# Optimization experiments

Hardware: AMD Instinct MI355X
Metric: run time of the kernel (lower is better)

Reference implementation:

```python
import jax, jax.numpy as jnp
import numpy as np

N_NODES = 50000
N_EDGES = 800000
IN_DIM = 128
HID_DIM = 64


def gcn_conv(x, W, b, src, dst, ew):
    """PyG GCNConv with edge_weight: add self-loops (weight 1), symmetric
    normalization D^-1/2 (A+I) D^-1/2, linear transform, scatter-add, bias."""
    n = x.shape[0]
    loop = jnp.arange(n)
    src_a = jnp.concatenate([src, loop])           # [E+N]
    dst_a = jnp.concatenate([dst, loop])
    ew_a = jnp.concatenate([ew, jnp.ones((n,), dtype=x.dtype)])
    deg = jax.ops.segment_sum(ew_a, dst_a, num_segments=n)   # [N]
    dinv = jnp.where(deg > 0, jax.lax.rsqrt(deg), 0.0)
    norm = dinv[src_a] * ew_a * dinv[dst_a]        # [E+N]
    h = x @ W                                      # [N, out]
    msg = h[src_a] * norm[:, None]                 # gather + scale
    out = jax.ops.segment_sum(msg, dst_a, num_segments=n)    # scatter-add
    return out + b


def setup_inputs() -> dict:
    key = jax.random.key(0)
    k = jax.random.split(key, 6)
    x = jax.random.normal(k[0], (N_NODES, IN_DIM), dtype=jnp.float32)
    edge_index = jax.random.randint(k[1], (2, N_EDGES), 0, N_NODES, dtype=jnp.int64)
    edge_weight = jax.random.uniform(k[2], (N_EDGES,), dtype=jnp.float32)
    W1 = jax.random.normal(k[3], (IN_DIM, HID_DIM), dtype=jnp.float32) * (1.0 / np.sqrt(IN_DIM))
    b1 = jnp.zeros((HID_DIM,), dtype=jnp.float32)
    W2 = jax.random.normal(k[4], (HID_DIM, 1), dtype=jnp.float32) * (1.0 / np.sqrt(HID_DIM))
    b2 = jnp.zeros((1,), dtype=jnp.float32)
    return {"x": x, "edge_index": edge_index, "edge_weight": edge_weight,
            "W1": W1, "b1": b1, "W2": W2, "b2": b2}


def reference(x, edge_index, edge_weight, W1, b1, W2, b2):
    src, dst = edge_index[0], edge_index[1]
    h = gcn_conv(x, W1, b1, src, dst, edge_weight)
    h = jax.nn.relu(h)
    h = gcn_conv(h, W2, b2, src, dst, edge_weight)
    return jax.nn.sigmoid(h).squeeze(-1)           # [N]
```

## Files before the change

### kernel.cpp

```cpp
#include <hip/hip_runtime.h>
#include <hip/hip_bf16.h>
#include <math.h>

#define N_NODES 50000
#define N_EDGES 800000
#define IN_DIM  128
#define HID_DIM 64

#define NBKT     196
#define BKT_CAP  5000
#define NPASSC   200
#define EDGES_PER_PASSC (N_EDGES / NPASSC)
#define GEMM_NODES 64
#define NGEMM    782
#define XS_LD    132

__global__ __launch_bounds__(256)
void partgemm_kernel(const int* __restrict__ src, const int* __restrict__ dst,
                     const float* __restrict__ ew, int* __restrict__ gcursor,
                     int2* __restrict__ edge_b,
                     const float* __restrict__ x, const float* __restrict__ W1,
                     __hip_bfloat16* __restrict__ h1b) {
    __shared__ float w1s[IN_DIM * HID_DIM];
    __shared__ float xs[GEMM_NODES][XS_LD];
    int bid = blockIdx.x;
    int tid = threadIdx.x;
    if (bid < NPASSC) {
        int2*           epack = (int2*)w1s;
        unsigned short* ebkt  = (unsigned short*)&xs[0][0];
        int* cnt1    = (int*)(ebkt + EDGES_PER_PASSC);
        int* cnt2    = cnt1 + 256;
        int* runbase = cnt2 + 256;
        cnt1[tid] = 0; cnt2[tid] = 0;
        __syncthreads();
        int e0 = bid * EDGES_PER_PASSC;
        const int4*   s4p = (const int4*)(src + e0);
        const int4*   d4p = (const int4*)(dst + e0);
        const float4* w4p = (const float4*)(ew + e0);
#pragma unroll
        for (int it = 0; it < 4; ++it) {
            int q = tid + 256 * it;
            if (q < EDGES_PER_PASSC / 4) {
                int4   s4 = s4p[q];
                int4   d4 = d4p[q];
                float4 w4 = w4p[q];
                int i = q * 4;
                epack[i + 0] = make_int2(s4.x | ((d4.x & 255) << 16), __float_as_int(w4.x));
                epack[i + 1] = make_int2(s4.y | ((d4.y & 255) << 16), __float_as_int(w4.y));
                epack[i + 2] = make_int2(s4.z | ((d4.z & 255) << 16), __float_as_int(w4.z));
                epack[i + 3] = make_int2(s4.w | ((d4.w & 255) << 16), __float_as_int(w4.w));
                ebkt[i + 0] = (unsigned short)(d4.x >> 8);
                ebkt[i + 1] = (unsigned short)(d4.y >> 8);
                ebkt[i + 2] = (unsigned short)(d4.z >> 8);
                ebkt[i + 3] = (unsigned short)(d4.w >> 8);
                atomicAdd(&cnt1[d4.x >> 8], 1);
                atomicAdd(&cnt1[d4.y >> 8], 1);
                atomicAdd(&cnt1[d4.z >> 8], 1);
                atomicAdd(&cnt1[d4.w >> 8], 1);
            }
        }
        __syncthreads();
        if (tid < NBKT) {
            int c = cnt1[tid];
            runbase[tid] = (c > 0) ? atomicAdd(&gcursor[tid], c) : 0;
        }
        __syncthreads();
        for (int i = tid; i < EDGES_PER_PASSC; i += 256) {
            int b = ebkt[i];
            int lr = atomicAdd(&cnt2[b], 1);
            edge_b[b * BKT_CAP + runbase[b] + lr] = epack[i];
        }
        return;
    }
    int gb = bid - NPASSC;
    int node0 = gb * GEMM_NODES;
    const float4* W4 = (const float4*)W1;
    float4* w1s4 = (float4*)w1s;
#pragma unroll
    for (int i = 0; i < 8; ++i) w1s4[tid + 256 * i] = W4[tid + 256 * i];
    {
        int r = tid >> 2, q = tid & 3;
        int row = node0 + r;
        if (row >= N_NODES) row = N_NODES - 1;
        const float4* xr = (const float4*)(x + (long)row * IN_DIM + q * 32);
#pragma unroll
        for (int i = 0; i < 8; ++i)
            *(float4*)&xs[r][q * 32 + i * 4] = xr[i];
    }
    __syncthreads();
    int w    = tid >> 6;
    int lane = tid & 63;
    int ng   = lane >> 2;
    int jg   = lane & 3;
    int j0   = w * 16 + jg * 4;
    float acc[4][4] = {{0.f}};
#pragma unroll 2
    for (int k = 0; k < IN_DIM; k += 4) {
        float4 wr0 = *(const float4*)&w1s[(k + 0) * HID_DIM + j0];
        float4 wr1 = *(const float4*)&w1s[(k + 1) * HID_DIM + j0];
        float4 wr2 = *(const float4*)&w1s[(k + 2) * HID_DIM + j0];
        float4 wr3 = *(const float4*)&w1s[(k + 3) * HID_DIM + j0];
#pragma unroll
        for (int i = 0; i < 4; ++i) {
            float4 xv = *(const float4*)&xs[ng + 16 * i][k];
            acc[i][0] += xv.x * wr0.x + xv.y * wr1.x + xv.z * wr2.x + xv.w * wr3.x;
            acc[i][1] += xv.x * wr0.y + xv.y * wr1.y + xv.z * wr2.y + xv.w * wr3.y;
            acc[i][2] += xv.x * wr0.z + xv.y * wr1.z + xv.z * wr2.z + xv.w * wr3.z;
            acc[i][3] += xv.x * wr0.w + xv.y * wr1.w + xv.z * wr2.w + xv.w * wr3.w;
        }
    }
#pragma unroll
    for (int i = 0; i < 4; ++i) {
        int n = node0 + ng + 16 * i;
        if (n < N_NODES) {
            __hip_bfloat16 bf[4];
            bf[0] = __float2bfloat16(acc[i][0]);
            bf[1] = __float2bfloat16(acc[i][1]);
            bf[2] = __float2bfloat16(acc[i][2]);
            bf[3] = __float2bfloat16(acc[i][3]);
            *(uint2*)&h1b[(long)n * HID_DIM + j0] = *(uint2*)bf;
        }
    }
}

__global__ __launch_bounds__(1024)
void bsort_kernel(const int* __restrict__ gcursor, const int2* __restrict__ edge_b,
                  int2* __restrict__ edge_s, int* __restrict__ start_g,
                  int* __restrict__ cnt_g, float* __restrict__ dinv) {
    __shared__ int   cnt[256];
    __shared__ int   cnt2[256];
    __shared__ float deg[256];
    __shared__ int   sc[256];
    int b   = blockIdx.x;
    int tid = threadIdx.x;
    int M    = gcursor[b];
    int base = b * BKT_CAP;
    if (tid < 256) { cnt[tid] = 0; cnt2[tid] = 0; deg[tid] = 0.0f; }
    __syncthreads();
    for (int i = tid; i < M; i += 1024) {
        int2 e = edge_b[base + i];
        int ld = (e.x >> 16) & 255;
        atomicAdd(&cnt[ld], 1);
        atomicAdd(&deg[ld], __int_as_float(e.y));
    }
    __syncthreads();
    if (tid < 256) sc[tid] = cnt[tid];
    __syncthreads();
#pragma unroll
    for (int off = 1; off < 256; off <<= 1) {
        int t = (tid >= off && tid < 256) ? sc[tid - off] : 0;
        __syncthreads();
        if (tid < 256) sc[tid] += t;
        __syncthreads();
    }
    if (tid < 256) {
        int startL = sc[tid] - cnt[tid];
        int node = b * 256 + tid;
        if (node < N_NODES) {
            start_g[node] = base + startL;
            cnt_g[node]   = cnt[tid];
            dinv[node]    = rsqrtf(1.0f + deg[tid]);
        }
        sc[tid] = startL;
    }
    __syncthreads();
    for (int i = tid; i < M; i += 1024) {
        int2 e = edge_b[base + i];
        int ld = (e.x >> 16) & 255;
        int r = atomicAdd(&cnt2[ld], 1);
        edge_s[base + sc[ld] + r] = make_int2(e.x & 0xFFFF, e.y);
    }
}

__global__ void gather1_layer2_kernel(const int* __restrict__ start_g, const int* __restrict__ cnt_g,
                                      const int2* __restrict__ edge_s,
                                      const __hip_bfloat16* __restrict__ h1b,
                                      const float* __restrict__ dinv, const float* __restrict__ b1,
                                      const float* __restrict__ W2, float* __restrict__ h2s) {
    __shared__ int2 meta[4][64];
    int wave = (blockIdx.x * blockDim.x + threadIdx.x) >> 6;
    int wl = threadIdx.x >> 6;
    int lane = threadIdx.x & 63;
    if (wave >= N_NODES) return;
    int s0 = start_g[wave];
    int ctotal = cnt_g[wave];
    int c0 = (lane & 31) * 2;
    int half = lane >> 5;
    float accA = 0.f, accB = 0.f, accA2 = 0.f, accB2 = 0.f;
    for (int done = 0; done < ctotal; done += 64) {
        int cnt = ctotal - done;
        if (cnt > 64) cnt = 64;
        if (lane < cnt) {
            int2 m = edge_s[s0 + done + lane];
            float w = __int_as_float(m.y) * dinv[m.x];
            meta[wl][lane] = make_int2(m.x, __float_as_int(w));
        }
        __builtin_amdgcn_wave_barrier();
        int cnte = cnt & ~1;
        int j = 0;
        for (; j + 16 <= cnte; j += 16) {
            int2 m0 = meta[wl][j +  0 + half];
            int2 m1 = meta[wl][j +  2 + half];
            int2 m2 = meta[wl][j +  4 + half];
            int2 m3 = meta[wl][j +  6 + half];
            int2 m4 = meta[wl][j +  8 + half];
            int2 m5 = meta[wl][j + 10 + half];
            int2 m6 = meta[wl][j + 12 + half];
            int2 m7 = meta[wl][j + 14 + half];
            unsigned int p0 = *(const unsigned int*)&h1b[m0.x * HID_DIM + c0];
            unsigned int p1 = *(const unsigned int*)&h1b[m1.x * HID_DIM + c0];
            unsigned int p2 = *(const unsigned int*)&h1b[m2.x * HID_DIM + c0];
            unsigned int p3 = *(const unsigned int*)&h1b[m3.x * HID_DIM + c0];
            unsigned int p4 = *(const unsigned int*)&h1b[m4.x * HID_DIM + c0];
            unsigned int p5 = *(const unsigned int*)&h1b[m5.x * HID_DIM + c0];
            unsigned int p6 = *(const unsigned int*)&h1b[m6.x * HID_DIM + c0];
            unsigned int p7 = *(const unsigned int*)&h1b[m7.x * HID_DIM + c0];
            float w0 = __int_as_float(m0.y), w1 = __int_as_float(m1.y);
            float w2 = __int_as_float(m2.y), w3 = __int_as_float(m3.y);
            float w4 = __int_as_float(m4.y), w5 = __int_as_float(m5.y);
            float w6 = __int_as_float(m6.y), w7 = __int_as_float(m7.y);
            accA  += w0 * __uint_as_float(p0 << 16);
            accB  += w0 * __uint_as_float(p0 & 0xFFFF0000u);
            accA2 += w1 * __uint_as_float(p1 << 16);
            accB2 += w1 * __uint_as_float(p1 & 0xFFFF0000u);
            accA  += w2 * __uint_as_float(p2 << 16);
            accB  += w2 * __uint_as_float(p2 & 0xFFFF0000u);
            accA2 += w3 * __uint_as_float(p3 << 16);
            accB2 += w3 * __uint_as_float(p3 & 0xFFFF0000u);
            accA  += w4 * __uint_as_float(p4 << 16);
            accB  += w4 * __uint_as_float(p4 & 0xFFFF0000u);
            accA2 += w5 * __uint_as_float(p5 << 16);
            accB2 += w5 * __uint_as_float(p5 & 0xFFFF0000u);
            accA  += w6 * __uint_as_float(p6 << 16);
            accB  += w6 * __uint_as_float(p6 & 0xFFFF0000u);
            accA2 += w7 * __uint_as_float(p7 << 16);
            accB2 += w7 * __uint_as_float(p7 & 0xFFFF0000u);
        }
        for (; j + 2 <= cnte; j += 2) {
            int2 m = meta[wl][j + half];
            unsigned int p = *(const unsigned int*)&h1b[m.x * HID_DIM + c0];
            accA += __int_as_float(m.y) * __uint_as_float(p << 16);
            accB += __int_as_float(m.y) * __uint_as_float(p & 0xFFFF0000u);
        }
        if ((cnt & 1) && half == 0) {
            int2 m = meta[wl][cnt - 1];
            unsigned int p = *(const unsigned int*)&h1b[m.x * HID_DIM + c0];
            accA += __int_as_float(m.y) * __uint_as_float(p << 16);
            accB += __int_as_float(m.y) * __uint_as_float(p & 0xFFFF0000u);
        }
        __builtin_amdgcn_wave_barrier();
    }
    accA += accA2; accB += accB2;
    accA += __shfl_xor(accA, 32, 64);
    accB += __shfl_xor(accB, 32, 64);
    float di = dinv[wave];
    unsigned int sp = *(const unsigned int*)&h1b[wave * HID_DIM + c0];
    float s0f = __uint_as_float(sp << 16);
    float s1f = __uint_as_float(sp & 0xFFFF0000u);
    float z0 = di * (accA + di * s0f) + b1[c0];
    float z1 = di * (accB + di * s1f) + b1[c0 + 1];
    float h0  = fmaxf(z0, 0.0f);
    float h1v = fmaxf(z1, 0.0f);
    float v = h0 * W2[c0] + h1v * W2[c0 + 1];
#pragma unroll
    for (int off = 16; off > 0; off >>= 1)
        v += __shfl_down(v, off, 32);
    if (lane == 0) h2s[wave] = v * di;
}

__global__ void gather2_final_kernel(const int* __restrict__ start_g, const int* __restrict__ cnt_g,
                                     const int2* __restrict__ edge_s,
                                     const float* __restrict__ h2s, const float* __restrict__ dinv,
                                     const float* __restrict__ b2, float* __restrict__ out) {
    int t = blockIdx.x * blockDim.x + threadIdx.x;
    int n = t >> 4;
    int sub = t & 15;
    if (n >= N_NODES) return;
    int s0 = start_g[n];
    int cnt = cnt_g[n];
    float acc = 0.0f;
    for (int j = sub; j < cnt; j += 16) {
        int2 m = edge_s[s0 + j];
        acc += __int_as_float(m.y) * h2s[m.x];
    }
#pragma unroll
    for (int off = 8; off > 0; off >>= 1)
        acc += __shfl_down(acc, off, 16);
    if (sub == 0) {
        float z = dinv[n] * (acc + h2s[n]) + b2[0];
        out[n] = 1.0f / (1.0f + expf(-z));
    }
}

extern "C" void kernel_launch(void* const* d_in, const int* in_sizes, int n_in,
                              void* d_out, int out_size, void* d_ws, size_t ws_size,
                              hipStream_t stream) {
    const float* x  = (const float*)d_in[0];
    const int*   ei = (const int*)d_in[1];
    const float* ew = (const float*)d_in[2];
    const float* W1 = (const float*)d_in[3];
    const float* b1 = (const float*)d_in[4];
    const float* W2 = (const float*)d_in[5];
    const float* b2 = (const float*)d_in[6];
    float* out = (float*)d_out;

    const int* src = ei;
    const int* dst = ei + N_EDGES;

    char* ws = (char*)d_ws;
    int2*  edge_b  = (int2*)ws;              ws += (size_t)NBKT * BKT_CAP * sizeof(int2);
    int2*  edge_s  = (int2*)ws;              ws += (size_t)NBKT * BKT_CAP * sizeof(int2);
    int*   gcursor = (int*)ws;               ws += NBKT * sizeof(int);
    int*   start_g = (int*)ws;               ws += N_NODES * sizeof(int);
    int*   cnt_g   = (int*)ws;               ws += N_NODES * sizeof(int);
    float* dinv    = (float*)ws;             ws += N_NODES * sizeof(float);
    float* h2s     = (float*)ws;             ws += N_NODES * sizeof(float);
    ws = (char*)(((uintptr_t)ws + 127) & ~(uintptr_t)127);
    __hip_bfloat16* h1b = (__hip_bfloat16*)ws;

    hipMemsetAsync(gcursor, 0, NBKT * sizeof(int), stream);
    partgemm_kernel<<<NPASSC + NGEMM, 256, 0, stream>>>(src, dst, ew, gcursor, edge_b, x, W1, h1b);
    bsort_kernel<<<NBKT, 1024, 0, stream>>>(gcursor, edge_b, edge_s, start_g, cnt_g, dinv);
    gather1_layer2_kernel<<<(N_NODES * 64) / 256, 256, 0, stream>>>(start_g, cnt_g, edge_s, h1b, dinv, b1, W2, h2s);
    gather2_final_kernel<<<(N_NODES * 16 + 255) / 256, 256, 0, stream>>>(start_g, cnt_g, edge_s, h2s, dinv, b2, out);
}
```

Baseline: 152.6 us.

## Locally sort edge partitions before scatter and vectorize bucket-sort loads

In the partition phase, each block now counting-sorts its edges by bucket in shared memory, via a prefix scan and a position-to-original index array. It then writes edges to the global bucket arrays in sorted order, so consecutive threads store to contiguous addresses instead of scattered ones. The bucket-sort kernel now reads edges two at a time with int4 loads and handles an odd tail separately. This adds an extra scan, extra barriers and more shared-memory traffic in exchange for coalesced global writes and wider reads. The int4 reinterpretation assumes the bucket base (b*BKT_CAP) keeps 16-byte alignment, which holds because BKT_CAP is even.

```diff
diff --git a/kernel.cpp b/kernel.cpp
--- a/kernel.cpp
+++ b/kernel.cpp
@@ -26,9 +26,10 @@
     int bid = blockIdx.x;
     int tid = threadIdx.x;
     if (bid < NPASSC) {
-        int2*           epack = (int2*)w1s;
-        unsigned short* ebkt  = (unsigned short*)&xs[0][0];
-        int* cnt1    = (int*)(ebkt + EDGES_PER_PASSC);
+        int2*           epack    = (int2*)w1s;
+        unsigned short* ebkt     = (unsigned short*)&xs[0][0];
+        unsigned short* pos2orig = ebkt + EDGES_PER_PASSC;
+        int* cnt1    = (int*)(pos2orig + EDGES_PER_PASSC);
         int* cnt2    = cnt1 + 256;
         int* runbase = cnt2 + 256;
         cnt1[tid] = 0; cnt2[tid] = 0;
@@ -60,15 +61,35 @@
             }
         }
         __syncthreads();
+        __shared__ int scuf[256];
+        scuf[tid] = cnt1[tid];
+        __syncthreads();
+#pragma unroll
+        for (int off = 1; off < 256; off <<= 1) {
+            int t = (tid >= off) ? scuf[tid - off] : 0;
+            __syncthreads();
+            scuf[tid] += t;
+            __syncthreads();
+        }
+        int runoff_t = scuf[tid] - cnt1[tid];
         if (tid < NBKT) {
             int c = cnt1[tid];
             runbase[tid] = (c > 0) ? atomicAdd(&gcursor[tid], c) : 0;
         }
         __syncthreads();
+        cnt1[tid] = runoff_t;
+        __syncthreads();
         for (int i = tid; i < EDGES_PER_PASSC; i += 256) {
             int b = ebkt[i];
             int lr = atomicAdd(&cnt2[b], 1);
-            edge_b[b * BKT_CAP + runbase[b] + lr] = epack[i];
+            pos2orig[cnt1[b] + lr] = (unsigned short)i;
+        }
+        __syncthreads();
+        for (int i = tid; i < EDGES_PER_PASSC; i += 256) {
+            int orig = pos2orig[i];
+            int2 e = epack[orig];
+            int b = ebkt[orig];
+            edge_b[b * BKT_CAP + runbase[b] + (i - cnt1[b])] = e;
         }
         return;
     }
@@ -137,8 +158,19 @@
     int base = b * BKT_CAP;
     if (tid < 256) { cnt[tid] = 0; cnt2[tid] = 0; deg[tid] = 0.0f; }
     __syncthreads();
-    for (int i = tid; i < M; i += 1024) {
-        int2 e = edge_b[base + i];
+    const int4* eb4 = (const int4*)(edge_b + base);
+    int Mh = M >> 1;
+    for (int i = tid; i < Mh; i += 1024) {
+        int4 p = eb4[i];
+        int ld0 = (p.x >> 16) & 255;
+        int ld1 = (p.z >> 16) & 255;
+        atomicAdd(&cnt[ld0], 1);
+        atomicAdd(&deg[ld0], __int_as_float(p.y));
+        atomicAdd(&cnt[ld1], 1);
+        atomicAdd(&deg[ld1], __int_as_float(p.w));
+    }
+    if (tid == 0 && (M & 1)) {
+        int2 e = edge_b[base + M - 1];
         int ld = (e.x >> 16) & 255;
         atomicAdd(&cnt[ld], 1);
         atomicAdd(&deg[ld], __int_as_float(e.y));
@@ -164,8 +196,17 @@
         sc[tid] = startL;
     }
     __syncthreads();
-    for (int i = tid; i < M; i += 1024) {
-        int2 e = edge_b[base + i];
+    for (int i = tid; i < Mh; i += 1024) {
+        int4 p = eb4[i];
+        int ld0 = (p.x >> 16) & 255;
+        int r0 = atomicAdd(&cnt2[ld0], 1);
+        edge_s[base + sc[ld0] + r0] = make_int2(p.x & 0xFFFF, p.y);
+        int ld1 = (p.z >> 16) & 255;
+        int r1 = atomicAdd(&cnt2[ld1], 1);
+        edge_s[base + sc[ld1] + r1] = make_int2(p.z & 0xFFFF, p.w);
+    }
+    if (tid == 0 && (M & 1)) {
+        int2 e = edge_b[base + M - 1];
         int ld = (e.x >> 16) & 255;
         int r = atomicAdd(&cnt2[ld], 1);
         edge_s[base + sc[ld] + r] = make_int2(e.x & 0xFFFF, e.y);
```

Result: no change. 151.4 us (-0.8%).
